# Kernel optimization log

Measured on AMD Instinct MI355X. Metric: run time of the kernel, lower is better.

## Reference

```python
import jax, jax.numpy as jnp
import numpy as np

D_MODEL = 1024
N_HEADS = 16
N_KV = 8
GROUP = N_HEADS // N_KV  # 2
D_HEAD = D_MODEL // N_HEADS  # 64
SCALE = D_HEAD ** -0.5


def setup_inputs() -> dict:
    key = jax.random.key(0)
    ks = jax.random.split(key, 5)
    s = 0.02
    return {
        "x": jax.random.normal(ks[0], (2, 2048, D_MODEL), dtype=jnp.float32),
        "Wq": jax.random.normal(ks[1], (D_MODEL, D_MODEL), dtype=jnp.float32) * s,
        "Wk": jax.random.normal(ks[2], (N_KV * D_HEAD, D_MODEL), dtype=jnp.float32) * s,
        "Wv": jax.random.normal(ks[3], (N_KV * D_HEAD, D_MODEL), dtype=jnp.float32) * s,
        "Wproj": jax.random.normal(ks[4], (D_MODEL, D_MODEL), dtype=jnp.float32) * s,
    }


def reference(x, Wq, Wk, Wv, Wproj):
    b, t, c = x.shape
    # projections (torch Linear: x @ W.T)
    q = (x @ Wq.T).reshape(b, t, N_KV, GROUP, D_HEAD)  # heads ordered (kv, group)
    k = (x @ Wk.T).reshape(b, t, N_KV, D_HEAD)
    v = (x @ Wv.T).reshape(b, t, N_KV, D_HEAD)
    # repeat_interleave(K/V, group, dim=heads) == broadcast over the group axis,
    # since q head index h maps to kv head h // GROUP.
    scores = jnp.einsum('btkgd,bskd->bkgts', q, k) * SCALE  # (b, kv, g, t, s)
    attn = jax.nn.softmax(scores, axis=-1)
    y = jnp.einsum('bkgts,bskd->btkgd', attn, v)  # (b, t, kv, g, d)
    y = y.reshape(b, t, c)
    return y @ Wproj.T
```

## Files before the change

kernel.cpp:

```cpp
#include <hip/hip_runtime.h>


#define SEQ    2048
#define CDIM   1024
#define KVDIM  512
#define SCL2E  0.18033688011112042f

typedef __attribute__((ext_vector_type(8))) short   bf16x8;
typedef __attribute__((ext_vector_type(4))) float   f32x4;
typedef unsigned short ushort_t;

__device__ __forceinline__ ushort_t f2bf(float f) {
    unsigned u = __float_as_uint(f);
    u += 0x7FFFu + ((u >> 16) & 1u);
    return (ushort_t)(u >> 16);
}
__device__ __forceinline__ float bf2f(ushort_t h) {
    return __uint_as_float(((unsigned)h) << 16);
}
__device__ __forceinline__ void load_lds16(const void* g, void* l) {
    __builtin_amdgcn_global_load_lds(
        (const __attribute__((address_space(1))) void*)g,
        (__attribute__((address_space(3))) void*)l, 16, 0, 0);
}

__global__ __launch_bounds__(256) void cvt_bf16(
    const float* __restrict__ x,  const float* __restrict__ wq,
    const float* __restrict__ wk, const float* __restrict__ wv,
    const float* __restrict__ wp,
    ushort_t* __restrict__ xh,  ushort_t* __restrict__ wqh,
    ushort_t* __restrict__ wkh, ushort_t* __restrict__ wvh,
    ushort_t* __restrict__ wph)
{
    const int i = blockIdx.x * 256 + threadIdx.x;
    const float* src; ushort_t* dst; int off;
    if (i < 1048576)      { src = x;  dst = xh;  off = i; }
    else if (i < 1310720) { src = wq; dst = wqh; off = i - 1048576; }
    else if (i < 1441792) { src = wk; dst = wkh; off = i - 1310720; }
    else if (i < 1572864) { src = wv; dst = wvh; off = i - 1441792; }
    else                  { src = wp; dst = wph; off = i - 1572864; }
    const float4 v = ((const float4*)src)[off];
    ushort4 h;
    h.x = f2bf(v.x); h.y = f2bf(v.y); h.z = f2bf(v.z); h.w = f2bf(v.w);
    ((ushort4*)dst)[off] = h;
}

__global__ __launch_bounds__(256, 4) void gemm64(
    const ushort_t* __restrict__ A, int K,
    const ushort_t* __restrict__ B1, void* __restrict__ C1, int N1, int epi1, float sc1,
    const ushort_t* __restrict__ B2, void* __restrict__ C2, int N2, int epi2, float sc2,
    const ushort_t* __restrict__ B3, void* __restrict__ C3, int N3, int epi3, float sc3)
{
    __shared__ ushort_t sA[128 * 64];
    __shared__ ushort_t sB[64 * 64];

    const int tid = threadIdx.x, wv = tid >> 6, lane = tid & 63;
    const int lm = lane & 15, quad = lane >> 4;
    const int m0 = blockIdx.y * 128;

    const int t1 = N1 >> 6, t2 = N2 >> 6;
    const int bx = blockIdx.x;
    const ushort_t* B; void* Cv; int n0, Nout, epi; float sc;
    if (bx < t1)           { B = B1; Cv = C1; Nout = N1; epi = epi1; sc = sc1; n0 = bx * 64; }
    else if (bx < t1 + t2) { B = B2; Cv = C2; Nout = N2; epi = epi2; sc = sc2; n0 = (bx - t1) * 64; }
    else                   { B = B3; Cv = C3; Nout = N3; epi = epi3; sc = sc3; n0 = (bx - t1 - t2) * 64; }

    const int mh = wv >> 1, nh = wv & 1;
    const int srow = lane >> 3;
    const int scol = ((lane & 7) ^ ((lane >> 3) & 7)) * 8;

    f32x4 acc[4][2] = {};

    for (int k0 = 0; k0 < K; k0 += 64) {
        __syncthreads();
        #pragma unroll
        for (int i = 0; i < 6; ++i) {
            const int g = wv * 6 + i;
            if (g < 16)
                load_lds16(A + (size_t)(m0 + g * 8 + srow) * K + k0 + scol, sA + g * 512);
            else
                load_lds16(B + (size_t)(n0 + (g - 16) * 8 + srow) * K + k0 + scol, sB + (g - 16) * 512);
        }
        __syncthreads();

        #pragma unroll
        for (int ks = 0; ks < 2; ++ks) {
            const int co = ((ks * 4 + quad) ^ (lm & 7)) * 8;
            bf16x8 a[4], b[2];
            #pragma unroll
            for (int mt = 0; mt < 4; ++mt)
                a[mt] = *(const bf16x8*)&sA[(mh * 64 + mt * 16 + lm) * 64 + co];
            #pragma unroll
            for (int nt = 0; nt < 2; ++nt)
                b[nt] = *(const bf16x8*)&sB[(nh * 32 + nt * 16 + lm) * 64 + co];
            #pragma unroll
            for (int mt = 0; mt < 4; ++mt)
                #pragma unroll
                for (int nt = 0; nt < 2; ++nt)
                    acc[mt][nt] = __builtin_amdgcn_mfma_f32_16x16x32_bf16(a[mt], b[nt], acc[mt][nt], 0, 0, 0);
        }
    }

    if (epi == 0) {
        float* C = (float*)Cv;
        #pragma unroll
        for (int mt = 0; mt < 4; ++mt)
            #pragma unroll
            for (int nt = 0; nt < 2; ++nt)
                #pragma unroll
                for (int r = 0; r < 4; ++r)
                    C[(size_t)(m0 + mh * 64 + mt * 16 + quad * 4 + r) * Nout + n0 + nh * 32 + nt * 16 + lm]
                        = acc[mt][nt][r];
    } else if (epi == 2) {
        ushort_t* C = (ushort_t*)Cv;
        const int bB   = m0 >> 11;
        const int tloc = (m0 & 2047) + mh * 64 + quad * 4;
        #pragma unroll
        for (int mt = 0; mt < 4; ++mt)
            #pragma unroll
            for (int nt = 0; nt < 2; ++nt) {
                const int n = n0 + nh * 32 + nt * 16 + lm;
                ushort4 u;
                u.x = f2bf(acc[mt][nt][0]);
                u.y = f2bf(acc[mt][nt][1]);
                u.z = f2bf(acc[mt][nt][2]);
                u.w = f2bf(acc[mt][nt][3]);
                *(ushort4*)&C[(size_t)(bB * KVDIM + n) * SEQ + tloc + mt * 16] = u;
            }
    } else {
        ushort_t* C = (ushort_t*)Cv;
        #pragma unroll
        for (int mt = 0; mt < 4; ++mt)
            #pragma unroll
            for (int nt = 0; nt < 2; ++nt)
                #pragma unroll
                for (int r = 0; r < 4; ++r)
                    C[(size_t)(m0 + mh * 64 + mt * 16 + quad * 4 + r) * Nout + n0 + nh * 32 + nt * 16 + lm]
                        = f2bf(acc[mt][nt][r] * sc);
    }
}

__global__ __launch_bounds__(256, 2) void attn4(
    const ushort_t* __restrict__ Qh, const ushort_t* __restrict__ Kh,
    const ushort_t* __restrict__ Vth, ushort_t* __restrict__ Yh)
{
    __shared__ ushort_t sK[2][128 * 64];
    __shared__ ushort_t sV[2][64 * 128];

    const int tid = threadIdx.x, wv = tid >> 6, lane = tid & 63;
    const int lm = lane & 15, quad = lane >> 4;
    const int b = blockIdx.y >> 4, h = blockIdx.y & 15, kvh = h >> 1;
    const int t0 = blockIdx.x * 128, tq0 = t0 + wv * 32;

    bf16x8 qh[2][2];
    #pragma unroll
    for (int qg = 0; qg < 2; ++qg) {
        const size_t rb = (size_t)(b * SEQ + tq0 + qg * 16 + lm) * CDIM + h * 64;
        #pragma unroll
        for (int ks = 0; ks < 2; ++ks)
            qh[qg][ks] = *(const bf16x8*)(Qh + rb + ks * 32 + quad * 8);
    }

    const ushort_t* gK = Kh  + (size_t)b * SEQ * KVDIM + kvh * 64;
    const ushort_t* gV = Vth + (size_t)(b * 8 + kvh) * 64 * SEQ;

    const int g0 = (wv & 1) * 8;

    const int srow = lane >> 3;
    const int scol = ((lane & 7) ^ ((lane >> 3) & 7)) * 8;

    int krow[8];
    #pragma unroll
    for (int it = 0; it < 8; ++it) {
        const int lr = (g0 + it) * 8 + srow;
        krow[it] = (lr & 0x60) | ((lr & 0x10) >> 2) | ((lr & 0x0C) << 1) | (lr & 3);
    }

    const int vrow = lane >> 4;
    const int vpos = lane & 15;

    float l_a[2] = {0.0f, 0.0f}, l_b[2] = {0.0f, 0.0f};
    f32x4 O[2][4] = {};

    if (wv < 2) {
        #pragma unroll
        for (int it = 0; it < 8; ++it)
            load_lds16(gK + (size_t)krow[it] * KVDIM + scol,
                       &sK[0][(g0 + it) * 512]);
    } else {
        #pragma unroll
        for (int it = 0; it < 8; ++it) {
            const int d = (g0 + it) * 4 + vrow;
            load_lds16(gV + (size_t)d * SEQ + (vpos ^ (d & 7)) * 8,
                       &sV[0][(g0 + it) * 512]);
        }
    }

    typedef union { bf16x8 v; unsigned u[4]; } pku;

    for (int kt = 0; kt < SEQ / 128; ++kt) {
        const int cur = kt & 1;
        __syncthreads();

        if (kt + 1 < SEQ / 128) {
            const int s1 = (kt + 1) * 128;
            if (wv < 2) {
                #pragma unroll
                for (int it = 0; it < 8; ++it)
                    load_lds16(gK + (size_t)(s1 + krow[it]) * KVDIM + scol,
                               &sK[cur ^ 1][(g0 + it) * 512]);
            } else {
                #pragma unroll
                for (int it = 0; it < 8; ++it) {
                    const int d = (g0 + it) * 4 + vrow;
                    load_lds16(gV + (size_t)d * SEQ + s1 + (vpos ^ (d & 7)) * 8,
                               &sV[cur ^ 1][(g0 + it) * 512]);
                }
            }
        }

        f32x4 st[2][8] = {};
        __builtin_amdgcn_s_setprio(1);
        #pragma unroll
        for (int sti = 0; sti < 8; ++sti)
            #pragma unroll
            for (int ks = 0; ks < 2; ++ks) {
                const int off = (sti * 16 + lm) * 64 + (((ks * 4 + quad) ^ (lm & 7)) * 8);
                const bf16x8 kf = *(const bf16x8*)&sK[cur][off];
                #pragma unroll
                for (int qg = 0; qg < 2; ++qg)
                    st[qg][sti] = __builtin_amdgcn_mfma_f32_16x16x32_bf16(kf, qh[qg][ks], st[qg][sti], 0, 0, 0);
            }
        __builtin_amdgcn_s_setprio(0);

        pku pa[2][4];
        #pragma unroll
        for (int qg = 0; qg < 2; ++qg)
            #pragma unroll
            for (int sti = 0; sti < 8; ++sti) {
                const float p0 = __builtin_amdgcn_exp2f(st[qg][sti][0]);
                const float p1 = __builtin_amdgcn_exp2f(st[qg][sti][1]);
                const float p2 = __builtin_amdgcn_exp2f(st[qg][sti][2]);
                const float p3 = __builtin_amdgcn_exp2f(st[qg][sti][3]);
                if (sti & 1) l_b[qg] += (p0 + p1) + (p2 + p3);
                else         l_a[qg] += (p0 + p1) + (p2 + p3);
                pa[qg][sti >> 1].u[(sti & 1) * 2 + 0] =
                    __builtin_amdgcn_perm(__float_as_uint(p1), __float_as_uint(p0), 0x07060302u);
                pa[qg][sti >> 1].u[(sti & 1) * 2 + 1] =
                    __builtin_amdgcn_perm(__float_as_uint(p3), __float_as_uint(p2), 0x07060302u);
            }

        __builtin_amdgcn_s_setprio(1);
        #pragma unroll
        for (int ks = 0; ks < 4; ++ks) {
            const int co = ((ks * 4 + quad) ^ (lm & 7)) * 8;
            #pragma unroll
            for (int dt = 0; dt < 4; ++dt) {
                const bf16x8 vt = *(const bf16x8*)&sV[cur][(dt * 16 + lm) * 128 + co];
                #pragma unroll
                for (int qg = 0; qg < 2; ++qg)
                    O[qg][dt] = __builtin_amdgcn_mfma_f32_16x16x32_bf16(pa[qg][ks].v, vt, O[qg][dt], 0, 0, 0);
            }
        }
        __builtin_amdgcn_s_setprio(0);
    }

    float l_r[2];
    #pragma unroll
    for (int qg = 0; qg < 2; ++qg) {
        l_r[qg] = l_a[qg] + l_b[qg];
        l_r[qg] += __shfl_xor(l_r[qg], 16);
        l_r[qg] += __shfl_xor(l_r[qg], 32);
    }
    #pragma unroll
    for (int qg = 0; qg < 2; ++qg)
        #pragma unroll
        for (int r = 0; r < 4; ++r) {
            const float lq = __shfl(l_r[qg], (lane & 48) | (quad * 4 + r));
            const float inv = 1.0f / lq;
            const int t = tq0 + qg * 16 + quad * 4 + r;
            const size_t rowb = (size_t)(b * SEQ + t) * CDIM + h * 64;
            #pragma unroll
            for (int dt = 0; dt < 4; ++dt)
                Yh[rowb + dt * 16 + lm] = f2bf(O[qg][dt][r] * inv);
        }
}

extern "C" void kernel_launch(void* const* d_in, const int* in_sizes, int n_in,
                              void* d_out, int out_size, void* d_ws, size_t ws_size,
                              hipStream_t stream)
{
    const float* x     = (const float*)d_in[0];
    const float* Wq    = (const float*)d_in[1];
    const float* Wk    = (const float*)d_in[2];
    const float* Wv    = (const float*)d_in[3];
    const float* Wproj = (const float*)d_in[4];
    float* out = (float*)d_out;

    const int M = 2 * SEQ;

    char* p = (char*)d_ws;
    ushort_t* xh   = (ushort_t*)p; p += (size_t)M * CDIM * 2;
    ushort_t* wqh  = (ushort_t*)p; p += (size_t)CDIM * CDIM * 2;
    ushort_t* wkh  = (ushort_t*)p; p += (size_t)KVDIM * CDIM * 2;
    ushort_t* wvh  = (ushort_t*)p; p += (size_t)KVDIM * CDIM * 2;
    ushort_t* wph  = (ushort_t*)p; p += (size_t)CDIM * CDIM * 2;
    ushort_t* qh   = (ushort_t*)p; p += (size_t)M * CDIM * 2;
    ushort_t* kh   = (ushort_t*)p; p += (size_t)M * KVDIM * 2;
    ushort_t* vth  = (ushort_t*)p; p += (size_t)M * KVDIM * 2;
    ushort_t* yh = xh;

    dim3 blk(256);

    cvt_bf16<<<dim3(7168), blk, 0, stream>>>(
        x, Wq, Wk, Wv, Wproj, xh, wqh, wkh, wvh, wph);

    gemm64<<<dim3(32, 32), blk, 0, stream>>>(
        xh, CDIM,
        wqh, qh,  CDIM,  3, SCL2E,
        wkh, kh,  KVDIM, 3, 1.0f,
        wvh, vth, KVDIM, 2, 1.0f);

    attn4<<<dim3(SEQ / 128, 32), blk, 0, stream>>>(qh, kh, vth, yh);

    gemm64<<<dim3(16, 32), blk, 0, stream>>>(
        yh, CDIM,
        wph, out, CDIM, 0, 1.0f,
        nullptr, nullptr, 0, 0, 1.0f,
        nullptr, nullptr, 0, 0, 1.0f);
}
```

Before: 159.9 us.

## Double-buffer LDS tiles in gemm64 to overlap global loads with MFMA

The projection GEMM now keeps two LDS buffers for the A and B tiles. It issues the asynchronous global-to-LDS loads for the next K tile before computing on the current one, and drops one of the two barriers per iteration. The goal is to hide global memory latency behind the MFMA work. In exchange LDS use doubles and the launch bound falls from 4 to 3 blocks per CU, which cuts occupancy. The compiler may also insert conservative waits that serialize the loads again.

Result: slower. 168.5 us (+5.4%).

```diff
diff --git a/kernel.cpp b/kernel.cpp
--- a/kernel.cpp
+++ b/kernel.cpp
@@ -45,14 +45,14 @@
     ((ushort4*)dst)[off] = h;
 }
 
-__global__ __launch_bounds__(256, 4) void gemm64(
+__global__ __launch_bounds__(256, 3) void gemm64(
     const ushort_t* __restrict__ A, int K,
     const ushort_t* __restrict__ B1, void* __restrict__ C1, int N1, int epi1, float sc1,
     const ushort_t* __restrict__ B2, void* __restrict__ C2, int N2, int epi2, float sc2,
     const ushort_t* __restrict__ B3, void* __restrict__ C3, int N3, int epi3, float sc3)
 {
-    __shared__ ushort_t sA[128 * 64];
-    __shared__ ushort_t sB[64 * 64];
+    __shared__ ushort_t sA[2][128 * 64];
+    __shared__ ushort_t sB[2][64 * 64];
 
     const int tid = threadIdx.x, wv = tid >> 6, lane = tid & 63;
     const int lm = lane & 15, quad = lane >> 4;
@@ -69,19 +69,35 @@
     const int srow = lane >> 3;
     const int scol = ((lane & 7) ^ ((lane >> 3) & 7)) * 8;
 
+    const int gbase = wv * 6;
+
     f32x4 acc[4][2] = {};
 
-    for (int k0 = 0; k0 < K; k0 += 64) {
+    #pragma unroll
+    for (int i = 0; i < 6; ++i) {
+        const int g = gbase + i;
+        if (g < 16)
+            load_lds16(A + (size_t)(m0 + g * 8 + srow) * K + scol, &sA[0][g * 512]);
+        else
+            load_lds16(B + (size_t)(n0 + (g - 16) * 8 + srow) * K + scol, &sB[0][(g - 16) * 512]);
+    }
+
+    const int nk = K >> 6;
+    for (int kt = 0; kt < nk; ++kt) {
+        const int cur = kt & 1;
         __syncthreads();
-        #pragma unroll
-        for (int i = 0; i < 6; ++i) {
-            const int g = wv * 6 + i;
-            if (g < 16)
-                load_lds16(A + (size_t)(m0 + g * 8 + srow) * K + k0 + scol, sA + g * 512);
-            else
-                load_lds16(B + (size_t)(n0 + (g - 16) * 8 + srow) * K + k0 + scol, sB + (g - 16) * 512);
-        }
-        __syncthreads();
+
+        if (kt + 1 < nk) {
+            const int k1 = (kt + 1) * 64;
+            #pragma unroll
+            for (int i = 0; i < 6; ++i) {
+                const int g = gbase + i;
+                if (g < 16)
+                    load_lds16(A + (size_t)(m0 + g * 8 + srow) * K + k1 + scol, &sA[cur ^ 1][g * 512]);
+                else
+                    load_lds16(B + (size_t)(n0 + (g - 16) * 8 + srow) * K + k1 + scol, &sB[cur ^ 1][(g - 16) * 512]);
+            }
+        }
 
         #pragma unroll
         for (int ks = 0; ks < 2; ++ks) {
@@ -89,10 +105,10 @@
             bf16x8 a[4], b[2];
             #pragma unroll
             for (int mt = 0; mt < 4; ++mt)
-                a[mt] = *(const bf16x8*)&sA[(mh * 64 + mt * 16 + lm) * 64 + co];
+                a[mt] = *(const bf16x8*)&sA[cur][(mh * 64 + mt * 16 + lm) * 64 + co];
             #pragma unroll
             for (int nt = 0; nt < 2; ++nt)
-                b[nt] = *(const bf16x8*)&sB[(nh * 32 + nt * 16 + lm) * 64 + co];
+                b[nt] = *(const bf16x8*)&sB[cur][(nh * 32 + nt * 16 + lm) * 64 + co];
             #pragma unroll
             for (int mt = 0; mt < 4; ++mt)
                 #pragma unroll
```
